# Optimization experiments

Hardware: AMD Instinct MI355X
Metric: run time of the kernel (lower is better)

## Reference

```python
import jax, jax.numpy as jnp
import numpy as np

B, L, HS = 32, 128, 512
P, M = 12, 1024
V, D = 50000, 128
P_TOTAL = 16
CHAR_LEN, CHAR_V = 16, 100
PRI_POS = (0, 1, 2, 3)  # privacy POS tags
TEMP = 1.0              # eval-mode temperature


def setup_inputs() -> dict:
    key = jax.random.key(0)
    ks = jax.random.split(key, 16)
    return {
        "ctx": jax.random.normal(ks[0], (B, L, HS), jnp.float32),
        "dec_W": jax.random.normal(ks[1], (P, HS, M), jnp.float32) * 0.05,
        "dec_b": jax.random.normal(ks[2], (P, M), jnp.float32) * 0.05,
        "psr_weight": jax.random.normal(ks[3], (V, D), jnp.float32),
        "atk_weight": jax.random.normal(ks[4], (V, D), jnp.float32),
        "cpy_W1": jax.random.normal(ks[5], (HS, 64), jnp.float32) * 0.05,
        "cpy_b1": jax.random.normal(ks[6], (64,), jnp.float32) * 0.05,
        "cpy_W2": jax.random.normal(ks[7], (64, 2), jnp.float32) * 0.05,
        "cpy_b2": jax.random.normal(ks[8], (2,), jnp.float32) * 0.05,
        "inp_word": jax.random.randint(ks[9], (B, L), 0, V),
        "inp_pos": jax.random.randint(ks[10], (B, L), 0, P_TOTAL),
        "inp_mask": jnp.ones((B, L), jnp.int32),
        "words": jax.random.randint(ks[11], (P, M), 0, V),
        "lut": jax.random.randint(ks[12], (V, CHAR_LEN), 0, CHAR_V),
    }


def _gumbel_softmax_hard(logits, key, t):
    # hard (straight-through) gumbel-softmax; forward value is one-hot
    u = jax.random.uniform(key, logits.shape, logits.dtype, 1e-6, 1.0 - 1e-6)
    g = -jnp.log(-jnp.log(u))
    y = jax.nn.softmax((logits + g) / t, axis=-1)
    idx = jnp.argmax(y, axis=-1)
    y_hard = jax.nn.one_hot(idx, logits.shape[-1], dtype=y.dtype)
    return y_hard + y - jax.lax.stop_gradient(y), idx


def reference(ctx, dec_W, dec_b, psr_weight, atk_weight,
              cpy_W1, cpy_b1, cpy_W2, cpy_b2,
              inp_word, inp_pos, inp_mask, words, lut):
    bs, ls = inp_word.shape
    N = bs * ls
    gkey = jax.random.key(42)

    ctx_f = ctx.reshape(N, -1)                      # [N, HS]
    pos_f = inp_pos.reshape(N)
    word_f = inp_word.reshape(N)

    ori_psr = psr_weight[word_f]                    # [N, D] gather
    ori_atk = atk_weight[word_f]
    obf_word = word_f
    obf_psr = ori_psr
    obf_atk = ori_atk
    obf_mask = jnp.zeros((N,), bool)
    pri_mask = jnp.zeros((N,), bool)
    entropy = jnp.float32(0.0)

    for p in range(P):  # small fixed set of POS tags (structurally distinct decoders)
        m = pos_f == p                              # [N] routing mask
        obf_mask = obf_mask | m
        if p in PRI_POS:
            pri_mask = pri_mask | m
        cnt = jnp.sum(m.astype(jnp.int32))
        logp = jax.nn.log_softmax(ctx_f @ dec_W[p] + dec_b[p], axis=-1)  # [N, M]
        ent_elem = -logp * jnp.exp(logp)
        ent_p = jnp.sum(jnp.where(m[:, None], ent_elem, 0.0)) / jnp.maximum(cnt * M, 1).astype(jnp.float32)
        entropy = entropy + jnp.where(cnt > 0, ent_p, 0.0)
        spt, idx = _gumbel_softmax_hard(logp, jax.random.fold_in(gkey, p), TEMP)
        spt_word = words[p][idx]                    # map local id -> vocab id
        obf_word = jnp.where(m, spt_word, obf_word)
        psr_p = spt @ psr_weight[words[p]]          # [N, D], per-POS sub-table
        atk_p = spt @ atk_weight[words[p]]
        obf_psr = jnp.where(m[:, None], psr_p, obf_psr)
        obf_atk = jnp.where(m[:, None], atk_p, obf_atk)

    # copy classifier
    h = jax.nn.relu(ctx_f @ cpy_W1 + cpy_b1)
    pcpy = jax.nn.log_softmax(h @ cpy_W2 + cpy_b2, axis=-1)  # [N, 2]
    # do_not_copy_pri: force pcpy to [0, 1] on privacy tokens
    pcpy = jnp.where(pri_mask[:, None], jnp.array([0.0, 1.0], pcpy.dtype), pcpy)

    cpy, _ = _gumbel_softmax_hard(pcpy, jax.random.fold_in(gkey, 999), TEMP)  # [N, 2]
    mask_f = inp_mask.reshape(N).astype(bool)
    cpy_mask = (cpy[:, 0] == 1.0) & mask_f

    noroot = inp_mask.astype(bool).at[:, 0].set(False).reshape(N)
    nr_cnt = jnp.maximum(jnp.sum(noroot.astype(jnp.int32)), 1).astype(jnp.float32)
    logp2 = jax.nn.log_softmax(pcpy, axis=-1)       # F.cross_entropy applies log_softmax again
    cpy_loss = -jnp.sum(jnp.where(noroot, logp2[:, 1], 0.0)) / nr_cnt  # cpy_penalty = 1.0 (applied twice)

    # use_copy: blend original vs obfuscated via (hard) copy gate
    c0, c1 = cpy[:, 0:1], cpy[:, 1:2]
    psr_out = (ori_psr * c0 + obf_psr * c1).reshape(bs, ls, -1)
    atk_out = (ori_atk * c0 + obf_atk * c1).reshape(bs, ls, -1)
    obf_mask = obf_mask & ~cpy_mask
    out_word = (word_f.astype(jnp.float32) * cpy[:, 0]
                + obf_word.astype(jnp.float32) * cpy[:, 1]).astype(jnp.int32).reshape(bs, ls)

    obf_char = lut[out_word]                        # [B, L, CHAR_LEN]
    ent_loss = -entropy  # ent_penalty = 1.0

    return (out_word, obf_char, psr_out, atk_out,
            obf_mask.reshape(bs, ls), cpy_mask.reshape(bs, ls),
            pri_mask.reshape(bs, ls), cpy_loss, ent_loss)
```

## Files before the change

kernel.cpp:

```cpp
#include <hip/hip_runtime.h>
#include <math.h>

#define BB 32
#define LL 128
#define HSZ 512
#define PP 12
#define MM 1024
#define VV 50000
#define DD 128
#define CLEN 16
#define NTOT 4096

#define RT 64
#define CT 64
#define BK 64
#define PADW 68
#define LISTCAP 512

#define OFF_WORD  0
#define OFF_CHAR  4096
#define OFF_PSR   69632
#define OFF_ATK   593920
#define OFF_OBFM  1118208
#define OFF_CPYM  1122304
#define OFF_PRIM  1126400
#define OFF_CLOSS 1130496
#define OFF_ELOSS 1130497

#define WS_LOGITS_OFF 8192

__device__ __forceinline__ float EXP32(float x){ return (float)exp((double)x); }
__device__ __forceinline__ float LOG32(float x){ return (float)log((double)x); }

__device__ __forceinline__ unsigned rotl32(unsigned x, int r){ return (x<<r)|(x>>(32-r)); }
__device__ __forceinline__ void tf2x32(unsigned k0, unsigned k1, unsigned x0, unsigned x1,
                                       unsigned &o0, unsigned &o1){
  unsigned ks2 = k0 ^ k1 ^ 0x1BD11BDAu;
  x0 += k0; x1 += k1;
  x0+=x1; x1=rotl32(x1,13); x1^=x0;
  x0+=x1; x1=rotl32(x1,15); x1^=x0;
  x0+=x1; x1=rotl32(x1,26); x1^=x0;
  x0+=x1; x1=rotl32(x1, 6); x1^=x0;
  x0+=k1; x1+=ks2+1u;
  x0+=x1; x1=rotl32(x1,17); x1^=x0;
  x0+=x1; x1=rotl32(x1,29); x1^=x0;
  x0+=x1; x1=rotl32(x1,16); x1^=x0;
  x0+=x1; x1=rotl32(x1,24); x1^=x0;
  x0+=ks2; x1+=k0+2u;
  x0+=x1; x1=rotl32(x1,13); x1^=x0;
  x0+=x1; x1=rotl32(x1,15); x1^=x0;
  x0+=x1; x1=rotl32(x1,26); x1^=x0;
  x0+=x1; x1=rotl32(x1, 6); x1^=x0;
  x0+=k0; x1+=k1+3u;
  x0+=x1; x1=rotl32(x1,17); x1^=x0;
  x0+=x1; x1=rotl32(x1,29); x1^=x0;
  x0+=x1; x1=rotl32(x1,16); x1^=x0;
  x0+=x1; x1=rotl32(x1,24); x1^=x0;
  x0+=k1; x1+=ks2+4u;
  x0+=x1; x1=rotl32(x1,13); x1^=x0;
  x0+=x1; x1=rotl32(x1,15); x1^=x0;
  x0+=x1; x1=rotl32(x1,26); x1^=x0;
  x0+=x1; x1=rotl32(x1, 6); x1^=x0;
  x0+=ks2; x1+=k0+5u;
  o0=x0; o1=x1;
}

__device__ __forceinline__ unsigned tf_bits32(unsigned k0, unsigned k1, unsigned e){
  unsigned o0, o1; tf2x32(k0, k1, 0u, e, o0, o1); return o0 ^ o1;
}

__device__ __forceinline__ float bits_to_unif(unsigned bits){
  const float lo = 1e-6f;
  const float hi = (float)(1.0 - 1e-6);
  const float span = hi - lo;
  unsigned fb = (bits >> 9) | 0x3f800000u;
  float f = __fsub_rn(__uint_as_float(fb), 1.0f);
  float r = __fadd_rn(__fmul_rn(f, span), lo);
  return fmaxf(lo, r);
}

__device__ __forceinline__ float gumbel_from_bits(unsigned bits){
  float u = bits_to_unif(bits);
  float v = -LOG32(u);
  return -LOG32(v);
}

__global__ __launch_bounds__(256)
void build_idx(const int* __restrict__ inp_pos, int* __restrict__ cntg,
               int* __restrict__ rowlist)
{
  int n = blockIdx.x*256 + threadIdx.x;
  if (n < NTOT){
    int p = inp_pos[n];
    if (p < PP){
      int slot = atomicAdd(&cntg[p], 1);
      if (slot < LISTCAP) rowlist[p*LISTCAP + slot] = n;
    }
  }
}

__global__ __launch_bounds__(256)
void gemm_kernel(const float* __restrict__ ctx, const float* __restrict__ dec_W,
                 const int* __restrict__ cntg, const int* __restrict__ rowlist,
                 float* __restrict__ logits)
{
  const int p  = blockIdx.z;
  const int c0 = blockIdx.x * CT;
  const int r0 = blockIdx.y * RT;
  const int cnt0 = cntg[p];
  const int cnt  = cnt0 < LISTCAP ? cnt0 : LISTCAP;
  if (r0 >= cnt) return;
  const int t = threadIdx.x;

  __shared__ float As[BK][PADW];
  __shared__ float Bs[BK][PADW];
  __shared__ int   rid_s[RT];

  if (t < RT){
    int rr = r0 + t;
    rid_s[t] = rowlist[p*LISTCAP + (rr < cnt ? rr : cnt-1)];
  }
  __syncthreads();

  const int tr = t >> 4;
  const int tc = t & 15;

  double acc[4][4];
  #pragma unroll
  for (int i = 0; i < 4; ++i)
    #pragma unroll
    for (int j = 0; j < 4; ++j) acc[i][j] = 0.0;

  const float* Wp = dec_W + (size_t)p * HSZ * MM;

  for (int k0 = 0; k0 < HSZ; k0 += BK){
    #pragma unroll
    for (int i = 0; i < 4; ++i){
      int idx = t + i*256;
      int r = idx >> 4;
      int q = idx & 15;
      const float4 v = *(const float4*)(ctx + (size_t)rid_s[r]*HSZ + k0 + q*4);
      As[q*4+0][r] = v.x;
      As[q*4+1][r] = v.y;
      As[q*4+2][r] = v.z;
      As[q*4+3][r] = v.w;
    }
    #pragma unroll
    for (int i = 0; i < 4; ++i){
      int idx = t + i*256;
      int kk = idx >> 4;
      int q  = idx & 15;
      const float4 v = *(const float4*)(Wp + (size_t)(k0+kk)*MM + c0 + q*4);
      *(float4*)&Bs[kk][q*4] = v;
    }
    __syncthreads();
    #pragma unroll 4
    for (int kk = 0; kk < BK; ++kk){
      float4 af = *(const float4*)&As[kk][tr*4];
      float4 bf = *(const float4*)&Bs[kk][tc*4];
      double a0 = (double)af.x, a1 = (double)af.y, a2 = (double)af.z, a3 = (double)af.w;
      double b0 = (double)bf.x, b1 = (double)bf.y, b2 = (double)bf.z, b3 = (double)bf.w;
      acc[0][0]+=a0*b0; acc[0][1]+=a0*b1; acc[0][2]+=a0*b2; acc[0][3]+=a0*b3;
      acc[1][0]+=a1*b0; acc[1][1]+=a1*b1; acc[1][2]+=a1*b2; acc[1][3]+=a1*b3;
      acc[2][0]+=a2*b0; acc[2][1]+=a2*b1; acc[2][2]+=a2*b2; acc[2][3]+=a2*b3;
      acc[3][0]+=a3*b0; acc[3][1]+=a3*b1; acc[3][2]+=a3*b2; acc[3][3]+=a3*b3;
    }
    __syncthreads();
  }

  #pragma unroll
  for (int i = 0; i < 4; ++i){
    int rr = r0 + tr*4 + i;
    if (rr < cnt){
      int rg = rid_s[tr*4 + i];
      float4 o;
      o.x = (float)acc[i][0]; o.y = (float)acc[i][1];
      o.z = (float)acc[i][2]; o.w = (float)acc[i][3];
      *(float4*)(logits + (size_t)rg*MM + c0 + tc*4) = o;
    }
  }
}

__global__ __launch_bounds__(256)
void finalize_kernel(const float* __restrict__ ctx, const float* __restrict__ dec_b,
                     const float* __restrict__ psr_w, const float* __restrict__ atk_w,
                     const float* __restrict__ cW1, const float* __restrict__ cb1,
                     const float* __restrict__ cW2, const float* __restrict__ cb2,
                     const int* __restrict__ inp_word, const int* __restrict__ inp_pos,
                     const int* __restrict__ inp_mask, const int* __restrict__ words,
                     const int* __restrict__ lut, const float* __restrict__ logitsbuf,
                     float* __restrict__ out, float* __restrict__ ws)
{
  const int n = blockIdx.x;
  const int t = threadIdx.x;

  __shared__ float  ctx_s[HSZ];
  __shared__ float  logit_s[MM];
  __shared__ float  h_s[64];
  __shared__ double redd[256];
  __shared__ float  redf[256];
  __shared__ int    redi[256];
  __shared__ float  sc[2];
  __shared__ int    si[1];

  for (int k = t; k < HSZ; k += 256) ctx_s[k] = ctx[(size_t)n*HSZ + k];
  __syncthreads();

  const int  pos   = inp_pos[n];
  const int  word  = inp_word[n];
  const int  msk   = inp_mask[n];
  const bool isobf = (pos < PP);
  const bool ispri = (pos < 4);

  if (t < 64){
    double acc = 0.0;
    for (int k = 0; k < HSZ; ++k) acc += (double)ctx_s[k] * (double)cW1[k*64 + t];
    float hv = __fadd_rn((float)acc, cb1[t]);
    h_s[t] = hv > 0.f ? hv : 0.f;
  }
  __syncthreads();

  if (t == 0){
    double a0 = 0.0, a1 = 0.0;
    for (int k = 0; k < 64; ++k){
      double hv = (double)h_s[k];
      a0 += hv * (double)cW2[k*2 + 0];
      a1 += hv * (double)cW2[k*2 + 1];
    }
    float pc0 = __fadd_rn((float)a0, cb2[0]);
    float pc1 = __fadd_rn((float)a1, cb2[1]);
    float m2  = fmaxf(pc0, pc1);
    float s0  = __fsub_rn(pc0, m2), s1 = __fsub_rn(pc1, m2);
    float se  = __fadd_rn(EXP32(s0), EXP32(s1));
    float lse = LOG32(se);
    float q0  = __fsub_rn(s0, lse), q1 = __fsub_rn(s1, lse);
    if (ispri){ q0 = 0.0f; q1 = 1.0f; }

    unsigned k90, k91; tf2x32(0u, 42u, 0u, 999u, k90, k91);
    float g0 = gumbel_from_bits(tf_bits32(k90, k91, (unsigned)(2*n)));
    float g1 = gumbel_from_bits(tf_bits32(k90, k91, (unsigned)(2*n + 1)));

    float x0 = __fadd_rn(q0, g0), x1 = __fadd_rn(q1, g1);
    float mm = fmaxf(x0, x1);
    float ex0 = EXP32(__fsub_rn(x0, mm));
    float ex1 = EXP32(__fsub_rn(x1, mm));
    float ssum = __fadd_rn(ex0, ex1);
    float y0 = __fdiv_rn(ex0, ssum), y1 = __fdiv_rn(ex1, ssum);
    int   idx2 = (y1 > y0) ? 1 : 0;
    float ysel = idx2 ? y1 : y0;
    float c    = __fsub_rn(__fadd_rn(1.0f, ysel), ysel);
    sc[0] = (idx2 == 0) ? c : 0.0f;
    sc[1] = (idx2 == 1) ? c : 0.0f;

    float m3 = fmaxf(q0, q1);
    float t0 = __fsub_rn(q0, m3), t1 = __fsub_rn(q1, m3);
    float se2 = __fadd_rn(EXP32(t0), EXP32(t1));
    float l21 = __fsub_rn(t1, LOG32(se2));
    if (msk != 0 && (n & (LL-1)) != 0) atomicAdd(ws + 12, l21);
  }

  if (isobf){
    const int m0 = 4*t;
    const float4 lg = *(const float4*)(logitsbuf + (size_t)n*MM + m0);
    const float* bp = dec_b + (size_t)pos * MM;
    logit_s[m0+0] = __fadd_rn(lg.x, bp[m0+0]);
    logit_s[m0+1] = __fadd_rn(lg.y, bp[m0+1]);
    logit_s[m0+2] = __fadd_rn(lg.z, bp[m0+2]);
    logit_s[m0+3] = __fadd_rn(lg.w, bp[m0+3]);
    __syncthreads();

    float lm = logit_s[m0];
    lm = fmaxf(lm, logit_s[m0+1]); lm = fmaxf(lm, logit_s[m0+2]); lm = fmaxf(lm, logit_s[m0+3]);
    redf[t] = lm; __syncthreads();
    for (int s = 128; s > 0; s >>= 1){ if (t < s) redf[t] = fmaxf(redf[t], redf[t+s]); __syncthreads(); }
    const float xmax = redf[0];
    __syncthreads();

    double ds = 0.0;
    for (int j = 0; j < 4; ++j)
      ds += (double)EXP32(__fsub_rn(logit_s[m0+j], xmax));
    redd[t] = ds; __syncthreads();
    for (int s = 128; s > 0; s >>= 1){ if (t < s) redd[t] += redd[t+s]; __syncthreads(); }
    const float lse = LOG32((float)redd[0]);
    __syncthreads();

    unsigned kp0, kp1; tf2x32(0u, 42u, 0u, (unsigned)pos, kp0, kp1);

    float best = -3.4e38f; int bi = 0; double es = 0.0;
    for (int j = 0; j < 4; ++j){
      int m = m0 + j;
      float sh = __fsub_rn(logit_s[m], xmax);
      float lp = __fsub_rn(sh, lse);
      float ex = EXP32(lp);
      es += (double)__fmul_rn(-lp, ex);
      float g = gumbel_from_bits(tf_bits32(kp0, kp1, (unsigned)(n*MM + m)));
      float sv = __fadd_rn(lp, g);
      if (sv > best){ best = sv; bi = m; }
    }
    redf[t] = best; redi[t] = bi; redd[t] = es; __syncthreads();
    for (int s = 128; s > 0; s >>= 1){
      if (t < s){
        float v2 = redf[t+s]; int i2 = redi[t+s];
        if (v2 > redf[t] || (v2 == redf[t] && i2 < redi[t])){ redf[t] = v2; redi[t] = i2; }
        redd[t] += redd[t+s];
      }
      __syncthreads();
    }
    if (t == 0){ si[0] = redi[0]; atomicAdd(ws + pos, (float)redd[0]); }
    __syncthreads();
  } else {
    __syncthreads();
  }

  const int   idx = isobf ? si[0] : 0;
  const float c0 = sc[0], c1 = sc[1];
  const int   obf_word = isobf ? words[pos*MM + idx] : word;

  if (t == 0){
    float of = __fadd_rn(__fmul_rn((float)word, c0), __fmul_rn((float)obf_word, c1));
    int ow = (int)of;
    out[OFF_WORD + n] = (float)ow;
    bool cpym = (c0 == 1.0f) && (msk != 0);
    out[OFF_CPYM + n] = cpym ? 1.f : 0.f;
    out[OFF_OBFM + n] = (isobf && !cpym) ? 1.f : 0.f;
    out[OFF_PRIM + n] = ispri ? 1.f : 0.f;
    #pragma unroll
    for (int j = 0; j < CLEN; ++j)
      out[OFF_CHAR + (size_t)n*CLEN + j] = (float)lut[(size_t)ow*CLEN + j];
  }
  if (t < DD){
    float po = psr_w[(size_t)word*DD + t];
    float pb = isobf ? psr_w[(size_t)obf_word*DD + t] : po;
    out[OFF_PSR + (size_t)n*DD + t] = __fadd_rn(__fmul_rn(po, c0), __fmul_rn(pb, c1));
    float ao = atk_w[(size_t)word*DD + t];
    float ab = isobf ? atk_w[(size_t)obf_word*DD + t] : ao;
    out[OFF_ATK + (size_t)n*DD + t] = __fadd_rn(__fmul_rn(ao, c0), __fmul_rn(ab, c1));
  }
}

__global__ __launch_bounds__(256)
void row_kernel_mono(const float* __restrict__ ctx, const float* __restrict__ dec_W,
                const float* __restrict__ dec_b, const float* __restrict__ psr_w,
                const float* __restrict__ atk_w, const float* __restrict__ cW1,
                const float* __restrict__ cb1, const float* __restrict__ cW2,
                const float* __restrict__ cb2, const int* __restrict__ inp_word,
                const int* __restrict__ inp_pos, const int* __restrict__ inp_mask,
                const int* __restrict__ words, const int* __restrict__ lut,
                float* __restrict__ out, float* __restrict__ ws)
{
  const int n = blockIdx.x;
  const int t = threadIdx.x;

  __shared__ float  ctx_s[HSZ];
  __shared__ float  logit_s[MM];
  __shared__ float  h_s[64];
  __shared__ double redd[256];
  __shared__ float  redf[256];
  __shared__ int    redi[256];
  __shared__ float  sc[2];
  __shared__ int    si[1];

  for (int k = t; k < HSZ; k += 256) ctx_s[k] = ctx[(size_t)n*HSZ + k];
  __syncthreads();

  const int  pos   = inp_pos[n];
  const int  word  = inp_word[n];
  const int  msk   = inp_mask[n];
  const bool isobf = (pos < PP);
  const bool ispri = (pos < 4);

  if (t < 64){
    double acc = 0.0;
    for (int k = 0; k < HSZ; ++k) acc += (double)ctx_s[k] * (double)cW1[k*64 + t];
    float hv = __fadd_rn((float)acc, cb1[t]);
    h_s[t] = hv > 0.f ? hv : 0.f;
  }
  __syncthreads();

  if (t == 0){
    double a0 = 0.0, a1 = 0.0;
    for (int k = 0; k < 64; ++k){
      double hv = (double)h_s[k];
      a0 += hv * (double)cW2[k*2 + 0];
      a1 += hv * (double)cW2[k*2 + 1];
    }
    float pc0 = __fadd_rn((float)a0, cb2[0]);
    float pc1 = __fadd_rn((float)a1, cb2[1]);
    float m2  = fmaxf(pc0, pc1);
    float s0  = __fsub_rn(pc0, m2), s1 = __fsub_rn(pc1, m2);
    float se  = __fadd_rn(EXP32(s0), EXP32(s1));
    float lse = LOG32(se);
    float q0  = __fsub_rn(s0, lse), q1 = __fsub_rn(s1, lse);
    if (ispri){ q0 = 0.0f; q1 = 1.0f; }

    unsigned k90, k91; tf2x32(0u, 42u, 0u, 999u, k90, k91);
    float g0 = gumbel_from_bits(tf_bits32(k90, k91, (unsigned)(2*n)));
    float g1 = gumbel_from_bits(tf_bits32(k90, k91, (unsigned)(2*n + 1)));

    float x0 = __fadd_rn(q0, g0), x1 = __fadd_rn(q1, g1);
    float mm = fmaxf(x0, x1);
    float ex0 = EXP32(__fsub_rn(x0, mm));
    float ex1 = EXP32(__fsub_rn(x1, mm));
    float ssum = __fadd_rn(ex0, ex1);
    float y0 = __fdiv_rn(ex0, ssum), y1 = __fdiv_rn(ex1, ssum);
    int   idx2 = (y1 > y0) ? 1 : 0;
    float ysel = idx2 ? y1 : y0;
    float c    = __fsub_rn(__fadd_rn(1.0f, ysel), ysel);
    sc[0] = (idx2 == 0) ? c : 0.0f;
    sc[1] = (idx2 == 1) ? c : 0.0f;

    float m3 = fmaxf(q0, q1);
    float t0 = __fsub_rn(q0, m3), t1 = __fsub_rn(q1, m3);
    float se2 = __fadd_rn(EXP32(t0), EXP32(t1));
    float l21 = __fsub_rn(t1, LOG32(se2));
    if (msk != 0 && (n & (LL-1)) != 0) atomicAdd(ws + 12, l21);
  }

  if (isobf){
    const float4* W4 = (const float4*)(dec_W + (size_t)pos * HSZ * MM);
    double a0=0.0, a1=0.0, a2=0.0, a3=0.0;
    for (int k = 0; k < HSZ; ++k){
      double c = (double)ctx_s[k];
      float4 w = W4[(size_t)k*256 + t];
      a0 += c*(double)w.x; a1 += c*(double)w.y; a2 += c*(double)w.z; a3 += c*(double)w.w;
    }
    const float* bp = dec_b + (size_t)pos * MM;
    const int m0 = 4*t;
    logit_s[m0+0] = __fadd_rn((float)a0, bp[m0+0]);
    logit_s[m0+1] = __fadd_rn((float)a1, bp[m0+1]);
    logit_s[m0+2] = __fadd_rn((float)a2, bp[m0+2]);
    logit_s[m0+3] = __fadd_rn((float)a3, bp[m0+3]);
    __syncthreads();

    float lm = logit_s[m0];
    lm = fmaxf(lm, logit_s[m0+1]); lm = fmaxf(lm, logit_s[m0+2]); lm = fmaxf(lm, logit_s[m0+3]);
    redf[t] = lm; __syncthreads();
    for (int s = 128; s > 0; s >>= 1){ if (t < s) redf[t] = fmaxf(redf[t], redf[t+s]); __syncthreads(); }
    const float xmax = redf[0];
    __syncthreads();

    double ds = 0.0;
    for (int j = 0; j < 4; ++j)
      ds += (double)EXP32(__fsub_rn(logit_s[m0+j], xmax));
    redd[t] = ds; __syncthreads();
    for (int s = 128; s > 0; s >>= 1){ if (t < s) redd[t] += redd[t+s]; __syncthreads(); }
    const float lse = LOG32((float)redd[0]);
    __syncthreads();

    unsigned kp0, kp1; tf2x32(0u, 42u, 0u, (unsigned)pos, kp0, kp1);

    float best = -3.4e38f; int bi = 0; double es = 0.0;
    for (int j = 0; j < 4; ++j){
      int m = m0 + j;
      float sh = __fsub_rn(logit_s[m], xmax);
      float lp = __fsub_rn(sh, lse);
      float ex = EXP32(lp);
      es += (double)__fmul_rn(-lp, ex);
      float g = gumbel_from_bits(tf_bits32(kp0, kp1, (unsigned)(n*MM + m)));
      float sv = __fadd_rn(lp, g);
      if (sv > best){ best = sv; bi = m; }
    }
    redf[t] = best; redi[t] = bi; redd[t] = es; __syncthreads();
    for (int s = 128; s > 0; s >>= 1){
      if (t < s){
        float v2 = redf[t+s]; int i2 = redi[t+s];
        if (v2 > redf[t] || (v2 == redf[t] && i2 < redi[t])){ redf[t] = v2; redi[t] = i2; }
        redd[t] += redd[t+s];
      }
      __syncthreads();
    }
    if (t == 0){ si[0] = redi[0]; atomicAdd(ws + pos, (float)redd[0]); }
    __syncthreads();
  } else {
    __syncthreads();
  }

  const int   idx = isobf ? si[0] : 0;
  const float c0 = sc[0], c1 = sc[1];
  const int   obf_word = isobf ? words[pos*MM + idx] : word;

  if (t == 0){
    float of = __fadd_rn(__fmul_rn((float)word, c0), __fmul_rn((float)obf_word, c1));
    int ow = (int)of;
    out[OFF_WORD + n] = (float)ow;
    bool cpym = (c0 == 1.0f) && (msk != 0);
    out[OFF_CPYM + n] = cpym ? 1.f : 0.f;
    out[OFF_OBFM + n] = (isobf && !cpym) ? 1.f : 0.f;
    out[OFF_PRIM + n] = ispri ? 1.f : 0.f;
    #pragma unroll
    for (int j = 0; j < CLEN; ++j)
      out[OFF_CHAR + (size_t)n*CLEN + j] = (float)lut[(size_t)ow*CLEN + j];
  }
  if (t < DD){
    float po = psr_w[(size_t)word*DD + t];
    float pb = isobf ? psr_w[(size_t)obf_word*DD + t] : po;
    out[OFF_PSR + (size_t)n*DD + t] = __fadd_rn(__fmul_rn(po, c0), __fmul_rn(pb, c1));
    float ao = atk_w[(size_t)word*DD + t];
    float ab = isobf ? atk_w[(size_t)obf_word*DD + t] : ao;
    out[OFF_ATK + (size_t)n*DD + t] = __fadd_rn(__fmul_rn(ao, c0), __fmul_rn(ab, c1));
  }
}

__global__ __launch_bounds__(256)
void fin_kernel(const int* __restrict__ inp_pos, const int* __restrict__ inp_mask,
                const float* __restrict__ ws, float* __restrict__ out)
{
  __shared__ int cnt[PP];
  __shared__ int nr;
  int t = threadIdx.x;
  if (t < PP) cnt[t] = 0;
  if (t == 0) nr = 0;
  __syncthreads();
  int ln = 0;
  for (int n = t; n < NTOT; n += 256){
    int p = inp_pos[n];
    if (p < PP) atomicAdd(&cnt[p], 1);
    if (inp_mask[n] != 0 && (n & (LL-1)) != 0) ln++;
  }
  atomicAdd(&nr, ln);
  __syncthreads();
  if (t == 0){
    float ent = 0.f;
    for (int p = 0; p < PP; ++p){
      int c = cnt[p];
      if (c > 0){
        int denom = c * MM; if (denom < 1) denom = 1;
        ent = __fadd_rn(ent, __fdiv_rn(ws[p], (float)denom));
      }
    }
    out[OFF_ELOSS] = -ent;
    int nrc = nr; if (nrc < 1) nrc = 1;
    out[OFF_CLOSS] = -__fdiv_rn(ws[12], (float)nrc);
  }
}

extern "C" void kernel_launch(void* const* d_in, const int* in_sizes, int n_in,
                              void* d_out, int out_size, void* d_ws, size_t ws_size,
                              hipStream_t stream)
{
  const float* ctx      = (const float*)d_in[0];
  const float* dec_W    = (const float*)d_in[1];
  const float* dec_b    = (const float*)d_in[2];
  const float* psr_w    = (const float*)d_in[3];
  const float* atk_w    = (const float*)d_in[4];
  const float* cW1      = (const float*)d_in[5];
  const float* cb1      = (const float*)d_in[6];
  const float* cW2      = (const float*)d_in[7];
  const float* cb2      = (const float*)d_in[8];
  const int*   inp_word = (const int*)d_in[9];
  const int*   inp_pos  = (const int*)d_in[10];
  const int*   inp_mask = (const int*)d_in[11];
  const int*   words    = (const int*)d_in[12];
  const int*   lut      = (const int*)d_in[13];
  float* out = (float*)d_out;
  float* ws  = (float*)d_ws;

  const size_t need = (size_t)WS_LOGITS_OFF*4 + (size_t)NTOT*MM*4;

  hipMemsetAsync(ws, 0, 512, stream);

  if (ws_size >= need){
    int*   cntg      = (int*)ws + 16;
    int*   rowlist   = (int*)ws + 64;
    float* logitsbuf = ws + WS_LOGITS_OFF;
    build_idx<<<NTOT/256, 256, 0, stream>>>(inp_pos, cntg, rowlist);
    gemm_kernel<<<dim3(MM/CT, LISTCAP/RT, PP), 256, 0, stream>>>(ctx, dec_W, cntg, rowlist, logitsbuf);
    finalize_kernel<<<NTOT, 256, 0, stream>>>(ctx, dec_b, psr_w, atk_w,
                                              cW1, cb1, cW2, cb2,
                                              inp_word, inp_pos, inp_mask, words, lut,
                                              logitsbuf, out, ws);
  } else {
    row_kernel_mono<<<NTOT, 256, 0, stream>>>(ctx, dec_W, dec_b, psr_w, atk_w,
                                              cW1, cb1, cW2, cb2,
                                              inp_word, inp_pos, inp_mask, words, lut,
                                              out, ws);
  }
  fin_kernel<<<1, 256, 0, stream>>>(inp_pos, inp_mask, ws, out);
}
```

Before: 392.2 us.

## Split copy-gate MLP into its own kernel, enlarge GEMM row tile, use wave reductions

The copy-gate MLP moves out of the finalize kernel into a separate cpy_kernel that spreads the 512-long dot products over all 256 threads instead of 64, and a shuffle reduction replaces the serial thread-0 loop. The gather GEMM now uses 128-row tiles with 8x4 double accumulators per thread and a row-major A tile, which drops the transposing scalar LDS stores. Finalize replaces its shared-memory tree reductions with wave shuffles plus a four-way cross-wave combine, and spreads the char-table writes across threads. The change adds a kernel launch and a workspace buffer, and the larger accumulator set raises register pressure in the double-precision GEMM.

```diff
diff --git a/kernel.cpp b/kernel.cpp
--- a/kernel.cpp
+++ b/kernel.cpp
@@ -11,10 +11,9 @@
 #define CLEN 16
 #define NTOT 4096
 
-#define RT 64
+#define RT 128
 #define CT 64
 #define BK 64
-#define PADW 68
 #define LISTCAP 512
 
 #define OFF_WORD  0
@@ -27,7 +26,8 @@
 #define OFF_CLOSS 1130496
 #define OFF_ELOSS 1130497
 
-#define WS_LOGITS_OFF 8192
+#define WS_SC_OFF     6656
+#define WS_LOGITS_OFF 16384
 
 __device__ __forceinline__ float EXP32(float x){ return (float)exp((double)x); }
 __device__ __forceinline__ float LOG32(float x){ return (float)log((double)x); }
@@ -100,6 +100,86 @@
 }
 
 __global__ __launch_bounds__(256)
+void cpy_kernel(const float* __restrict__ ctx, const float* __restrict__ cW1,
+                const float* __restrict__ cb1, const float* __restrict__ cW2,
+                const float* __restrict__ cb2, const int* __restrict__ inp_pos,
+                const int* __restrict__ inp_mask,
+                float* __restrict__ scbuf, float* __restrict__ ws)
+{
+  const int n = blockIdx.x;
+  const int t = threadIdx.x;
+  __shared__ float  ctxl[HSZ];
+  __shared__ double part[256];
+  __shared__ float  hsh[64];
+
+  if (t < 128) *(float4*)&ctxl[t*4] = *(const float4*)(ctx + (size_t)n*HSZ + t*4);
+  __syncthreads();
+
+  const int o = t & 63, seg = t >> 6;
+  {
+    double a = 0.0;
+    const float* w  = cW1 + (size_t)(seg*128)*64 + o;
+    const float* cs = ctxl + seg*128;
+    #pragma unroll 8
+    for (int kk = 0; kk < 128; ++kk) a += (double)cs[kk] * (double)w[kk*64];
+    part[t] = a;
+  }
+  __syncthreads();
+  if (t < 64){
+    double s = ((part[t] + part[64+t]) + part[128+t]) + part[192+t];
+    float hv = __fadd_rn((float)s, cb1[t]);
+    hsh[t] = hv > 0.f ? hv : 0.f;
+  }
+  __syncthreads();
+
+  if (t < 64){
+    double hd = (double)hsh[t];
+    double p0 = hd * (double)cW2[2*t + 0];
+    double p1 = hd * (double)cW2[2*t + 1];
+    #pragma unroll
+    for (int off = 32; off > 0; off >>= 1){
+      p0 += __shfl_xor(p0, off);
+      p1 += __shfl_xor(p1, off);
+    }
+    if (t == 0){
+      const int pos = inp_pos[n];
+      const int msk = inp_mask[n];
+      const bool ispri = (pos < 4);
+      float pc0 = __fadd_rn((float)p0, cb2[0]);
+      float pc1 = __fadd_rn((float)p1, cb2[1]);
+      float m2  = fmaxf(pc0, pc1);
+      float s0  = __fsub_rn(pc0, m2), s1 = __fsub_rn(pc1, m2);
+      float se  = __fadd_rn(EXP32(s0), EXP32(s1));
+      float lse = LOG32(se);
+      float q0  = __fsub_rn(s0, lse), q1 = __fsub_rn(s1, lse);
+      if (ispri){ q0 = 0.0f; q1 = 1.0f; }
+
+      unsigned k90, k91; tf2x32(0u, 42u, 0u, 999u, k90, k91);
+      float g0 = gumbel_from_bits(tf_bits32(k90, k91, (unsigned)(2*n)));
+      float g1 = gumbel_from_bits(tf_bits32(k90, k91, (unsigned)(2*n + 1)));
+
+      float x0 = __fadd_rn(q0, g0), x1 = __fadd_rn(q1, g1);
+      float mm = fmaxf(x0, x1);
+      float ex0 = EXP32(__fsub_rn(x0, mm));
+      float ex1 = EXP32(__fsub_rn(x1, mm));
+      float ssum = __fadd_rn(ex0, ex1);
+      float y0 = __fdiv_rn(ex0, ssum), y1 = __fdiv_rn(ex1, ssum);
+      int   idx2 = (y1 > y0) ? 1 : 0;
+      float ysel = idx2 ? y1 : y0;
+      float c    = __fsub_rn(__fadd_rn(1.0f, ysel), ysel);
+      scbuf[2*n + 0] = (idx2 == 0) ? c : 0.0f;
+      scbuf[2*n + 1] = (idx2 == 1) ? c : 0.0f;
+
+      float m3 = fmaxf(q0, q1);
+      float t0 = __fsub_rn(q0, m3), t1 = __fsub_rn(q1, m3);
+      float se2 = __fadd_rn(EXP32(t0), EXP32(t1));
+      float l21 = __fsub_rn(t1, LOG32(se2));
+      if (msk != 0 && (n & (LL-1)) != 0) atomicAdd(ws + 12, l21);
+    }
+  }
+}
+
+__global__ __launch_bounds__(256)
 void gemm_kernel(const float* __restrict__ ctx, const float* __restrict__ dec_W,
                  const int* __restrict__ cntg, const int* __restrict__ rowlist,
                  float* __restrict__ logits)
@@ -112,22 +192,22 @@
   if (r0 >= cnt) return;
   const int t = threadIdx.x;
 
-  __shared__ float As[BK][PADW];
-  __shared__ float Bs[BK][PADW];
+  __shared__ float As[RT][BK + 4];
+  __shared__ float Bs[BK][CT + 4];
   __shared__ int   rid_s[RT];
 
-  if (t < RT){
-    int rr = r0 + t;
-    rid_s[t] = rowlist[p*LISTCAP + (rr < cnt ? rr : cnt-1)];
+  for (int i = t; i < RT; i += 256){
+    int rr = r0 + i;
+    rid_s[i] = rowlist[p*LISTCAP + (rr < cnt ? rr : cnt-1)];
   }
   __syncthreads();
 
   const int tr = t >> 4;
   const int tc = t & 15;
 
-  double acc[4][4];
+  double acc[8][4];
   #pragma unroll
-  for (int i = 0; i < 4; ++i)
+  for (int i = 0; i < 8; ++i)
     #pragma unroll
     for (int j = 0; j < 4; ++j) acc[i][j] = 0.0;
 
@@ -135,44 +215,42 @@
 
   for (int k0 = 0; k0 < HSZ; k0 += BK){
     #pragma unroll
+    for (int i = 0; i < 8; ++i){
+      int s = t + i*256;
+      int r = s >> 4, q = s & 15;
+      float4 v = *(const float4*)(ctx + (size_t)rid_s[r]*HSZ + k0 + q*4);
+      *(float4*)&As[r][q*4] = v;
+    }
+    #pragma unroll
     for (int i = 0; i < 4; ++i){
-      int idx = t + i*256;
-      int r = idx >> 4;
-      int q = idx & 15;
-      const float4 v = *(const float4*)(ctx + (size_t)rid_s[r]*HSZ + k0 + q*4);
-      As[q*4+0][r] = v.x;
-      As[q*4+1][r] = v.y;
-      As[q*4+2][r] = v.z;
-      As[q*4+3][r] = v.w;
-    }
-    #pragma unroll
-    for (int i = 0; i < 4; ++i){
-      int idx = t + i*256;
-      int kk = idx >> 4;
-      int q  = idx & 15;
-      const float4 v = *(const float4*)(Wp + (size_t)(k0+kk)*MM + c0 + q*4);
+      int s = t + i*256;
+      int kk = s >> 4, q = s & 15;
+      float4 v = *(const float4*)(Wp + (size_t)(k0+kk)*MM + c0 + q*4);
       *(float4*)&Bs[kk][q*4] = v;
     }
     __syncthreads();
+
     #pragma unroll 4
     for (int kk = 0; kk < BK; ++kk){
-      float4 af = *(const float4*)&As[kk][tr*4];
       float4 bf = *(const float4*)&Bs[kk][tc*4];
-      double a0 = (double)af.x, a1 = (double)af.y, a2 = (double)af.z, a3 = (double)af.w;
       double b0 = (double)bf.x, b1 = (double)bf.y, b2 = (double)bf.z, b3 = (double)bf.w;
-      acc[0][0]+=a0*b0; acc[0][1]+=a0*b1; acc[0][2]+=a0*b2; acc[0][3]+=a0*b3;
-      acc[1][0]+=a1*b0; acc[1][1]+=a1*b1; acc[1][2]+=a1*b2; acc[1][3]+=a1*b3;
-      acc[2][0]+=a2*b0; acc[2][1]+=a2*b1; acc[2][2]+=a2*b2; acc[2][3]+=a2*b3;
-      acc[3][0]+=a3*b0; acc[3][1]+=a3*b1; acc[3][2]+=a3*b2; acc[3][3]+=a3*b3;
+      double a[8];
+      #pragma unroll
+      for (int i = 0; i < 8; ++i) a[i] = (double)As[tr*8 + i][kk];
+      #pragma unroll
+      for (int i = 0; i < 8; ++i){
+        acc[i][0] += a[i]*b0; acc[i][1] += a[i]*b1;
+        acc[i][2] += a[i]*b2; acc[i][3] += a[i]*b3;
+      }
     }
     __syncthreads();
   }
 
   #pragma unroll
-  for (int i = 0; i < 4; ++i){
-    int rr = r0 + tr*4 + i;
+  for (int i = 0; i < 8; ++i){
+    int rr = r0 + tr*8 + i;
     if (rr < cnt){
-      int rg = rid_s[tr*4 + i];
+      int rg = rid_s[tr*8 + i];
       float4 o;
       o.x = (float)acc[i][0]; o.y = (float)acc[i][1];
       o.z = (float)acc[i][2]; o.w = (float)acc[i][3];
@@ -182,152 +260,110 @@
 }
 
 __global__ __launch_bounds__(256)
-void finalize_kernel(const float* __restrict__ ctx, const float* __restrict__ dec_b,
+void finalize_kernel(const float* __restrict__ dec_b,
                      const float* __restrict__ psr_w, const float* __restrict__ atk_w,
-                     const float* __restrict__ cW1, const float* __restrict__ cb1,
-                     const float* __restrict__ cW2, const float* __restrict__ cb2,
                      const int* __restrict__ inp_word, const int* __restrict__ inp_pos,
                      const int* __restrict__ inp_mask, const int* __restrict__ words,
                      const int* __restrict__ lut, const float* __restrict__ logitsbuf,
+                     const float* __restrict__ scbuf,
                      float* __restrict__ out, float* __restrict__ ws)
 {
   const int n = blockIdx.x;
   const int t = threadIdx.x;
-
-  __shared__ float  ctx_s[HSZ];
-  __shared__ float  logit_s[MM];
-  __shared__ float  h_s[64];
-  __shared__ double redd[256];
-  __shared__ float  redf[256];
-  __shared__ int    redi[256];
-  __shared__ float  sc[2];
-  __shared__ int    si[1];
-
-  for (int k = t; k < HSZ; k += 256) ctx_s[k] = ctx[(size_t)n*HSZ + k];
-  __syncthreads();
+  const int wid = t >> 6, lane = t & 63;
+
+  __shared__ float  sMax[4];
+  __shared__ double sSum[4];
+  __shared__ double sEnt[4];
+  __shared__ float  sBv[4];
+  __shared__ int    sBi[4];
+  __shared__ int    si;
 
   const int  pos   = inp_pos[n];
   const int  word  = inp_word[n];
   const int  msk   = inp_mask[n];
   const bool isobf = (pos < PP);
   const bool ispri = (pos < 4);
-
-  if (t < 64){
-    double acc = 0.0;
-    for (int k = 0; k < HSZ; ++k) acc += (double)ctx_s[k] * (double)cW1[k*64 + t];
-    float hv = __fadd_rn((float)acc, cb1[t]);
-    h_s[t] = hv > 0.f ? hv : 0.f;
-  }
-  __syncthreads();
-
-  if (t == 0){
-    double a0 = 0.0, a1 = 0.0;
-    for (int k = 0; k < 64; ++k){
-      double hv = (double)h_s[k];
-      a0 += hv * (double)cW2[k*2 + 0];
-      a1 += hv * (double)cW2[k*2 + 1];
-    }
-    float pc0 = __fadd_rn((float)a0, cb2[0]);
-    float pc1 = __fadd_rn((float)a1, cb2[1]);
-    float m2  = fmaxf(pc0, pc1);
-    float s0  = __fsub_rn(pc0, m2), s1 = __fsub_rn(pc1, m2);
-    float se  = __fadd_rn(EXP32(s0), EXP32(s1));
-    float lse = LOG32(se);
-    float q0  = __fsub_rn(s0, lse), q1 = __fsub_rn(s1, lse);
-    if (ispri){ q0 = 0.0f; q1 = 1.0f; }
-
-    unsigned k90, k91; tf2x32(0u, 42u, 0u, 999u, k90, k91);
-    float g0 = gumbel_from_bits(tf_bits32(k90, k91, (unsigned)(2*n)));
-    float g1 = gumbel_from_bits(tf_bits32(k90, k91, (unsigned)(2*n + 1)));
-
-    float x0 = __fadd_rn(q0, g0), x1 = __fadd_rn(q1, g1);
-    float mm = fmaxf(x0, x1);
-    float ex0 = EXP32(__fsub_rn(x0, mm));
-    float ex1 = EXP32(__fsub_rn(x1, mm));
-    float ssum = __fadd_rn(ex0, ex1);
-    float y0 = __fdiv_rn(ex0, ssum), y1 = __fdiv_rn(ex1, ssum);
-    int   idx2 = (y1 > y0) ? 1 : 0;
-    float ysel = idx2 ? y1 : y0;
-    float c    = __fsub_rn(__fadd_rn(1.0f, ysel), ysel);
-    sc[0] = (idx2 == 0) ? c : 0.0f;
-    sc[1] = (idx2 == 1) ? c : 0.0f;
-
-    float m3 = fmaxf(q0, q1);
-    float t0 = __fsub_rn(q0, m3), t1 = __fsub_rn(q1, m3);
-    float se2 = __fadd_rn(EXP32(t0), EXP32(t1));
-    float l21 = __fsub_rn(t1, LOG32(se2));
-    if (msk != 0 && (n & (LL-1)) != 0) atomicAdd(ws + 12, l21);
-  }
+  const float c0 = scbuf[2*n + 0];
+  const float c1 = scbuf[2*n + 1];
 
   if (isobf){
     const int m0 = 4*t;
     const float4 lg = *(const float4*)(logitsbuf + (size_t)n*MM + m0);
-    const float* bp = dec_b + (size_t)pos * MM;
-    logit_s[m0+0] = __fadd_rn(lg.x, bp[m0+0]);
-    logit_s[m0+1] = __fadd_rn(lg.y, bp[m0+1]);
-    logit_s[m0+2] = __fadd_rn(lg.z, bp[m0+2]);
-    logit_s[m0+3] = __fadd_rn(lg.w, bp[m0+3]);
-    __syncthreads();
-
-    float lm = logit_s[m0];
-    lm = fmaxf(lm, logit_s[m0+1]); lm = fmaxf(lm, logit_s[m0+2]); lm = fmaxf(lm, logit_s[m0+3]);
-    redf[t] = lm; __syncthreads();
-    for (int s = 128; s > 0; s >>= 1){ if (t < s) redf[t] = fmaxf(redf[t], redf[t+s]); __syncthreads(); }
-    const float xmax = redf[0];
-    __syncthreads();
-
-    double ds = 0.0;
-    for (int j = 0; j < 4; ++j)
-      ds += (double)EXP32(__fsub_rn(logit_s[m0+j], xmax));
-    redd[t] = ds; __syncthreads();
-    for (int s = 128; s > 0; s >>= 1){ if (t < s) redd[t] += redd[t+s]; __syncthreads(); }
-    const float lse = LOG32((float)redd[0]);
-    __syncthreads();
+    const float4 bq = *(const float4*)(dec_b + (size_t)pos*MM + m0);
+    float l0 = __fadd_rn(lg.x, bq.x);
+    float l1 = __fadd_rn(lg.y, bq.y);
+    float l2 = __fadd_rn(lg.z, bq.z);
+    float l3 = __fadd_rn(lg.w, bq.w);
+
+    float lm = fmaxf(fmaxf(l0, l1), fmaxf(l2, l3));
+    #pragma unroll
+    for (int off = 32; off > 0; off >>= 1) lm = fmaxf(lm, __shfl_xor(lm, off));
+    if (lane == 0) sMax[wid] = lm;
+    __syncthreads();
+    const float xmax = fmaxf(fmaxf(sMax[0], sMax[1]), fmaxf(sMax[2], sMax[3]));
+
+    float e0 = EXP32(__fsub_rn(l0, xmax));
+    float e1 = EXP32(__fsub_rn(l1, xmax));
+    float e2 = EXP32(__fsub_rn(l2, xmax));
+    float e3 = EXP32(__fsub_rn(l3, xmax));
+    double ds = (((double)e0 + (double)e1) + (double)e2) + (double)e3;
+    #pragma unroll
+    for (int off = 32; off > 0; off >>= 1) ds += __shfl_xor(ds, off);
+    if (lane == 0) sSum[wid] = ds;
+    __syncthreads();
+    const double se = ((sSum[0] + sSum[1]) + sSum[2]) + sSum[3];
+    const float lse = LOG32((float)se);
+    const double inv_se = 1.0 / se;
 
     unsigned kp0, kp1; tf2x32(0u, 42u, 0u, (unsigned)pos, kp0, kp1);
-
     float best = -3.4e38f; int bi = 0; double es = 0.0;
+    float lv[4] = {l0, l1, l2, l3};
+    float ev[4] = {e0, e1, e2, e3};
+    #pragma unroll
     for (int j = 0; j < 4; ++j){
       int m = m0 + j;
-      float sh = __fsub_rn(logit_s[m], xmax);
+      float sh = __fsub_rn(lv[j], xmax);
       float lp = __fsub_rn(sh, lse);
-      float ex = EXP32(lp);
-      es += (double)__fmul_rn(-lp, ex);
+      es += (double)(-lp) * ((double)ev[j] * inv_se);
       float g = gumbel_from_bits(tf_bits32(kp0, kp1, (unsigned)(n*MM + m)));
       float sv = __fadd_rn(lp, g);
       if (sv > best){ best = sv; bi = m; }
     }
-    redf[t] = best; redi[t] = bi; redd[t] = es; __syncthreads();
-    for (int s = 128; s > 0; s >>= 1){
-      if (t < s){
-        float v2 = redf[t+s]; int i2 = redi[t+s];
-        if (v2 > redf[t] || (v2 == redf[t] && i2 < redi[t])){ redf[t] = v2; redi[t] = i2; }
-        redd[t] += redd[t+s];
-      }
-      __syncthreads();
-    }
-    if (t == 0){ si[0] = redi[0]; atomicAdd(ws + pos, (float)redd[0]); }
-    __syncthreads();
-  } else {
-    __syncthreads();
-  }
-
-  const int   idx = isobf ? si[0] : 0;
-  const float c0 = sc[0], c1 = sc[1];
+    #pragma unroll
+    for (int off = 32; off > 0; off >>= 1){
+      float ov = __shfl_xor(best, off);
+      int   oi = __shfl_xor(bi,   off);
+      if (ov > best || (ov == best && oi < bi)){ best = ov; bi = oi; }
+      es += __shfl_xor(es, off);
+    }
+    if (lane == 0){ sBv[wid] = best; sBi[wid] = bi; sEnt[wid] = es; }
+    __syncthreads();
+    if (t == 0){
+      float bv = sBv[0]; int b = sBi[0];
+      #pragma unroll
+      for (int w = 1; w < 4; ++w)
+        if (sBv[w] > bv || (sBv[w] == bv && sBi[w] < b)){ bv = sBv[w]; b = sBi[w]; }
+      si = b;
+      atomicAdd(ws + pos, (float)(((sEnt[0] + sEnt[1]) + sEnt[2]) + sEnt[3]));
+    }
+    __syncthreads();
+  }
+
+  const int   idx = isobf ? si : 0;
   const int   obf_word = isobf ? words[pos*MM + idx] : word;
 
+  float of = __fadd_rn(__fmul_rn((float)word, c0), __fmul_rn((float)obf_word, c1));
+  int ow = (int)of;
   if (t == 0){
-    float of = __fadd_rn(__fmul_rn((float)word, c0), __fmul_rn((float)obf_word, c1));
-    int ow = (int)of;
     out[OFF_WORD + n] = (float)ow;
     bool cpym = (c0 == 1.0f) && (msk != 0);
     out[OFF_CPYM + n] = cpym ? 1.f : 0.f;
     out[OFF_OBFM + n] = (isobf && !cpym) ? 1.f : 0.f;
     out[OFF_PRIM + n] = ispri ? 1.f : 0.f;
-    #pragma unroll
-    for (int j = 0; j < CLEN; ++j)
-      out[OFF_CHAR + (size_t)n*CLEN + j] = (float)lut[(size_t)ow*CLEN + j];
-  }
+  }
+  if (t < CLEN)
+    out[OFF_CHAR + (size_t)n*CLEN + t] = (float)lut[(size_t)ow*CLEN + t];
   if (t < DD){
     float po = psr_w[(size_t)word*DD + t];
     float pb = isobf ? psr_w[(size_t)obf_word*DD + t] : po;
@@ -555,20 +591,22 @@
   float* out = (float*)d_out;
   float* ws  = (float*)d_ws;
 
-  const size_t need = (size_t)WS_LOGITS_OFF*4 + (size_t)NTOT*MM*4;
+  const size_t need = ((size_t)WS_LOGITS_OFF + (size_t)NTOT*MM) * 4;
 
   hipMemsetAsync(ws, 0, 512, stream);
 
   if (ws_size >= need){
     int*   cntg      = (int*)ws + 16;
     int*   rowlist   = (int*)ws + 64;
+    float* scbuf     = ws + WS_SC_OFF;
     float* logitsbuf = ws + WS_LOGITS_OFF;
     build_idx<<<NTOT/256, 256, 0, stream>>>(inp_pos, cntg, rowlist);
+    cpy_kernel<<<NTOT, 256, 0, stream>>>(ctx, cW1, cb1, cW2, cb2,
+                                         inp_pos, inp_mask, scbuf, ws);
     gemm_kernel<<<dim3(MM/CT, LISTCAP/RT, PP), 256, 0, stream>>>(ctx, dec_W, cntg, rowlist, logitsbuf);
-    finalize_kernel<<<NTOT, 256, 0, stream>>>(ctx, dec_b, psr_w, atk_w,
-                                              cW1, cb1, cW2, cb2,
+    finalize_kernel<<<NTOT, 256, 0, stream>>>(dec_b, psr_w, atk_w,
                                               inp_word, inp_pos, inp_mask, words, lut,
-                                              logitsbuf, out, ws);
+                                              logitsbuf, scbuf, out, ws);
   } else {
     row_kernel_mono<<<NTOT, 256, 0, stream>>>(ctx, dec_W, dec_b, psr_w, atk_w,
                                               cW1, cb1, cW2, cb2,
```

After: 405.7 us. +3.5%, slower.
